# Kernel tuning notes

Hardware: AMD Instinct MI355X
Metric: run time of the kernel (lower is better)

Reference implementation:

```python
import jax, jax.numpy as jnp
import numpy as np

HEADS = 16
D_MODEL = 1024
IMG_MODEL = 512
D_K = D_MODEL // HEADS


def setup_inputs() -> dict:
    key = jax.random.key(0)
    ks = jax.random.split(key, 12)
    B, LQ, LKV = 8, 2048, 1024
    s_dm = 1.0 / np.sqrt(D_MODEL)
    s_im = 1.0 / np.sqrt(IMG_MODEL)
    return {
        "q": jax.random.normal(ks[0], (B, LQ, D_MODEL), jnp.float32),
        "k": jax.random.normal(ks[1], (B, LKV, IMG_MODEL), jnp.float32),
        "v": jax.random.normal(ks[2], (B, LKV, IMG_MODEL), jnp.float32),
        "Wq": jax.random.normal(ks[3], (D_MODEL, D_MODEL), jnp.float32) * s_dm,
        "bq": jnp.zeros((D_MODEL,), jnp.float32),
        "Wk": jax.random.normal(ks[4], (IMG_MODEL, D_MODEL), jnp.float32) * s_im,
        "bk": jnp.zeros((D_MODEL,), jnp.float32),
        "Wv": jax.random.normal(ks[5], (IMG_MODEL, D_MODEL), jnp.float32) * s_im,
        "bv": jnp.zeros((D_MODEL,), jnp.float32),
        "Wo": jax.random.normal(ks[6], (D_MODEL, D_MODEL), jnp.float32) * s_dm,
        "bo": jnp.zeros((D_MODEL,), jnp.float32),
    }


def reference(q, k, v, Wq, bq, Wk, bk, Wv, bv, Wo, bo):
    B, LQ, _ = q.shape
    LKV = k.shape[1]
    # projections -> [B, H, L, d_k]
    qh = (q @ Wq + bq).reshape(B, LQ, HEADS, D_K).transpose(0, 2, 1, 3)
    kh = (k @ Wk + bk).reshape(B, LKV, HEADS, D_K).transpose(0, 2, 1, 3)
    vh = (v @ Wv + bv).reshape(B, LKV, HEADS, D_K).transpose(0, 2, 1, 3)
    scale = 1.0 / np.sqrt(D_K)
    scores = jnp.einsum("bhqd,bhkd->bhqk", qh, kh) * scale  # [B,H,LQ,LKV]
    attn = jax.nn.softmax(scores, axis=-1)  # dropout = identity at eval
    out = jnp.einsum("bhqk,bhkd->bhqd", attn, vh)  # [B,H,LQ,d_k]
    concat = out.transpose(0, 2, 1, 3).reshape(B, LQ, D_MODEL)
    return concat @ Wo + bo
```

## Files before the change

kernel.cpp:

```cpp
#include <hip/hip_runtime.h>

typedef __bf16 bf16;
typedef __bf16 bf16x8 __attribute__((ext_vector_type(8)));
typedef __bf16 bf16x4 __attribute__((ext_vector_type(4)));
typedef float f32x4 __attribute__((ext_vector_type(4)));

constexpr int BB   = 8;
constexpr int LQ   = 2048;
constexpr int LKV  = 1024;
constexpr int DM   = 1024;
constexpr int DIMG = 512;
constexpr int H    = 16;
constexpr int DK   = 64;

__device__ inline void async16(const bf16* g, bf16* l) {
  __builtin_amdgcn_global_load_lds((const __attribute__((address_space(1))) void*)g,
                                   (__attribute__((address_space(3))) void*)l, 16, 0, 0);
}
__device__ inline float fexp2(float x) { return __builtin_amdgcn_exp2f(x); }

__global__ __launch_bounds__(256) void prep_all(const float* __restrict__ q,
                                                const float* __restrict__ k,
                                                const float* __restrict__ v,
                                                bf16* __restrict__ qo,
                                                bf16* __restrict__ ko,
                                                bf16* __restrict__ vo,
                                                int nq4, int nk4, int NC,
                                                const float* __restrict__ Wq,
                                                const float* __restrict__ Wk,
                                                const float* __restrict__ Wv,
                                                const float* __restrict__ Wo,
                                                bf16* __restrict__ WqT,
                                                bf16* __restrict__ WkT,
                                                bf16* __restrict__ WvT,
                                                bf16* __restrict__ WoT) {
  __shared__ float tile[64][65];
  const int bid = blockIdx.x;
  if (bid < NC) {
    int i = bid * 256 + threadIdx.x;
    const float* in;
    bf16* out;
    int idx;
    if (i < nq4) { in = q; out = qo; idx = i; }
    else if (i < nq4 + nk4) { in = k; out = ko; idx = i - nq4; }
    else if (i < nq4 + 2 * nk4) { in = v; out = vo; idx = i - nq4 - nk4; }
    else return;
    const float4 f = ((const float4*)in)[idx];
    bf16x4 o;
    o[0] = (bf16)f.x; o[1] = (bf16)f.y; o[2] = (bf16)f.z; o[3] = (bf16)f.w;
    ((bf16x4*)out)[idx] = o;
    return;
  }
  const int tbid = bid - NC;
  const int bx = tbid & 15, by = (tbid >> 4) & 15, z = tbid >> 8;
  const float* W;
  bf16* WT;
  int K;
  if (z == 0) { W = Wq; WT = WqT; K = DM; }
  else if (z == 1) { W = Wk; WT = WkT; K = DIMG; }
  else if (z == 2) { W = Wv; WT = WvT; K = DIMG; }
  else { W = Wo; WT = WoT; K = DM; }
  const int N = DM;
  if (bx * 64 >= K) return;

  const int k0 = bx * 64, n0 = by * 64;
  const int tx = threadIdx.x & 63, tg = threadIdx.x >> 6;
#pragma unroll
  for (int i = 0; i < 16; ++i) {
    int row = tg * 16 + i;
    tile[row][tx] = W[(size_t)(k0 + row) * N + n0 + tx];
  }
  __syncthreads();
#pragma unroll
  for (int i = 0; i < 16; ++i) {
    int nrow = tg * 16 + i;
    WT[(size_t)(n0 + nrow) * K + k0 + tx] = (bf16)tile[tx][nrow];
  }
}

template <typename OutT, bool VT_OUT>
__device__ __forceinline__ void gemm_body(const bf16* __restrict__ A,
                                          const bf16* __restrict__ Bt,
                                          const float* __restrict__ bias,
                                          OutT* __restrict__ C,
                                          int N, int K, float oscale, int bm, int bn,
                                          bf16* As, bf16* Bs) {
  const int tid = threadIdx.x, lane = tid & 63, wave = tid >> 6;
  const int wm = (wave & 1) * 64, wn = (wave >> 1) * 64;
  const int fm = lane & 15, quad = lane >> 4, fk8 = quad * 8;
  constexpr int SLOT = 128 * 32;

  f32x4 acc[4][4];
#pragma unroll
  for (int i = 0; i < 4; ++i)
#pragma unroll
    for (int j = 0; j < 4; ++j) {
      f32x4 z = {0.f, 0.f, 0.f, 0.f};
      acc[i][j] = z;
    }

  const int srow = lane >> 2, scol = (lane & 3) * 8;
  const bf16* ag0 = A + (size_t)(bm * 128 + wave * 16 + srow) * K + scol;
  const bf16* ag1 = ag0 + (size_t)64 * K;
  const bf16* bg0 = Bt + (size_t)(bn * 128 + wave * 16 + srow) * K + scol;
  const bf16* bg1 = bg0 + (size_t)64 * K;
  bf16* la0 = As + (wave * 16) * 32;
  bf16* la1 = As + (64 + wave * 16) * 32;
  bf16* lb0 = Bs + (wave * 16) * 32;
  bf16* lb1 = Bs + (64 + wave * 16) * 32;

  auto stage = [&](int t, int slot) {
    const int k0 = t * 32, so = slot * SLOT;
    async16(ag0 + k0, la0 + so);
    async16(ag1 + k0, la1 + so);
    async16(bg0 + k0, lb0 + so);
    async16(bg1 + k0, lb1 + so);
  };

  const int KT = K >> 5;
  stage(0, 0);
  stage(1, 1);

  for (int t = 0; t < KT; ++t) {
    asm volatile("s_waitcnt vmcnt(4)" ::: "memory");
    __builtin_amdgcn_s_barrier();
    __builtin_amdgcn_sched_barrier(0);
    {
      const int nt = t + 2;
      if (nt < KT) stage(nt, nt % 3);
      else if (nt == KT) stage(KT - 1, nt % 3);
    }
    const int cur = (t % 3) * SLOT;
    bf16x8 af[4], bfr[4];
#pragma unroll
    for (int i = 0; i < 4; ++i)
      af[i] = *(const bf16x8*)&As[cur + (wm + i * 16 + fm) * 32 + fk8];
#pragma unroll
    for (int j = 0; j < 4; ++j)
      bfr[j] = *(const bf16x8*)&Bs[cur + (wn + j * 16 + fm) * 32 + fk8];
#pragma unroll
    for (int i = 0; i < 4; ++i)
#pragma unroll
      for (int j = 0; j < 4; ++j)
        acc[i][j] = __builtin_amdgcn_mfma_f32_16x16x32_bf16(af[i], bfr[j], acc[i][j], 0, 0, 0);
  }
  asm volatile("s_waitcnt vmcnt(0)" ::: "memory");

#pragma unroll
  for (int j = 0; j < 4; ++j) {
    const int col = bn * 128 + wn + j * 16 + fm;
    const float bv = bias[col];
    if constexpr (VT_OUT) {
      const int h = col >> 6, dk = col & 63;
#pragma unroll
      for (int i = 0; i < 4; ++i) {
        const int row = bm * 128 + wm + i * 16 + quad * 4;
        const int b = row >> 10, t = row & 1023;
        bf16x4 o;
#pragma unroll
        for (int r = 0; r < 4; ++r) o[r] = (bf16)((acc[i][j][r] + bv) * oscale);
        *(bf16x4*)&C[(((size_t)(b * H + h) * DK + dk) << 10) + t] = o;
      }
    } else {
#pragma unroll
      for (int i = 0; i < 4; ++i) {
#pragma unroll
        for (int r = 0; r < 4; ++r) {
          const int row = bm * 128 + wm + i * 16 + quad * 4 + r;
          C[(size_t)row * N + col] = (OutT)((acc[i][j][r] + bv) * oscale);
        }
      }
    }
  }
}

template <typename OutT>
__global__ __launch_bounds__(256) void gemm_one(const bf16* __restrict__ A,
                                                const bf16* __restrict__ Bt,
                                                const float* __restrict__ bias,
                                                OutT* __restrict__ C,
                                                int N, int K, float oscale) {
  __shared__ __align__(16) bf16 As[3 * 128 * 32];
  __shared__ __align__(16) bf16 Bs[3 * 128 * 32];
  const int cpx = gridDim.x >> 3;
  const int wg = ((int)blockIdx.x & 7) * cpx + ((int)blockIdx.x >> 3);
  const int nbn = N >> 7;
  gemm_body<OutT, false>(A, Bt, bias, C, N, K, oscale, wg / nbn, wg % nbn, As, Bs);
}

__global__ __launch_bounds__(256) void gemm_qkv(const bf16* __restrict__ qbf,
                                                const bf16* __restrict__ WqT,
                                                const float* __restrict__ bq,
                                                bf16* __restrict__ qh,
                                                const bf16* __restrict__ kbf,
                                                const bf16* __restrict__ WkT,
                                                const float* __restrict__ bk,
                                                bf16* __restrict__ kh,
                                                const bf16* __restrict__ vbf,
                                                const bf16* __restrict__ WvT,
                                                const float* __restrict__ bv,
                                                bf16* __restrict__ Vt,
                                                float qscale) {
  __shared__ __align__(16) bf16 As[3 * 128 * 32];
  __shared__ __align__(16) bf16 Bs[3 * 128 * 32];
  const int cpx = gridDim.x >> 3;
  const int wg = ((int)blockIdx.x & 7) * cpx + ((int)blockIdx.x >> 3);
  if (wg < 1024) {
    gemm_body<bf16, false>(qbf, WqT, bq, qh, DM, DM, qscale, wg >> 3, wg & 7, As, Bs);
  } else if (wg < 1536) {
    const int idx = wg - 1024;
    gemm_body<bf16, false>(kbf, WkT, bk, kh, DM, DIMG, 1.0f, idx >> 3, idx & 7, As, Bs);
  } else {
    const int idx = wg - 1536;
    gemm_body<bf16, true>(vbf, WvT, bv, Vt, DM, DIMG, 1.0f, idx >> 3, idx & 7, As, Bs);
  }
}

__global__ __launch_bounds__(512, 4) void attn_kernel(const bf16* __restrict__ qh,
                                                      const bf16* __restrict__ kh,
                                                      const bf16* __restrict__ vt,
                                                      bf16* __restrict__ out) {
  constexpr int NT = LKV / 64;
  __shared__ __align__(16) bf16 Ks[2][64 * 64];
  __shared__ __align__(16) bf16 Vs[2][64 * 64];
  __shared__ __align__(16) bf16 Ps[8][32 * 64];

  const int tid = threadIdx.x, lane = tid & 63, w = tid >> 6;
  const int fm = lane & 15, quad = lane >> 4;
  const int qt = blockIdx.x, h = blockIdx.y, b = blockIdx.z;
  const int q0 = qt * 256;

  const bf16* qbase = qh + ((size_t)(b * LQ) + q0 + w * 32) * DM + h * DK;
  const bf16* kbase = kh + (size_t)(b * LKV) * DM + h * DK;
  const bf16* vbase = vt + (size_t)(b * H + h) * DK * LKV;

  bf16x8 qf[2][2];
#pragma unroll
  for (int i = 0; i < 2; ++i)
#pragma unroll
    for (int kg = 0; kg < 2; ++kg)
      qf[i][kg] = *(const bf16x8*)&qbase[(size_t)(i * 16 + fm) * DM + kg * 32 + quad * 8];

  const int srow = lane >> 3, sslot = lane & 7;
  const int fs = fm & 7;

  auto stage = [&](int t, int bf) {
    const int r0 = w * 8;
    const int row = r0 + srow;
    const int gs = (sslot ^ (row & 7)) << 3;
    async16(kbase + (size_t)(t * 64 + row) * DM + gs, &Ks[bf][r0 * 64]);
    async16(vbase + (size_t)row * LKV + t * 64 + gs, &Vs[bf][r0 * 64]);
  };

  stage(0, 0);
  stage(1, 1);

  float row_m[2] = {-1e30f, -1e30f}, row_l[2] = {0.f, 0.f};
  f32x4 o_acc[2][4];
#pragma unroll
  for (int i = 0; i < 2; ++i)
#pragma unroll
    for (int jd = 0; jd < 4; ++jd) {
      f32x4 z = {0.f, 0.f, 0.f, 0.f};
      o_acc[i][jd] = z;
    }

  bf16* Pw = Ps[w];

#pragma unroll 2
  for (int t = 0; t < NT; ++t) {
    asm volatile("s_waitcnt vmcnt(2)" ::: "memory");
    __builtin_amdgcn_s_barrier();
    __builtin_amdgcn_sched_barrier(0);
    const bf16* Kb = Ks[t & 1];
    const bf16* Vb = Vs[t & 1];

    f32x4 s[4][2];
#pragma unroll
    for (int m = 0; m < 4; ++m)
#pragma unroll
      for (int i = 0; i < 2; ++i) {
        f32x4 z = {0.f, 0.f, 0.f, 0.f};
        s[m][i] = z;
      }
    __builtin_amdgcn_s_setprio(1);
#pragma unroll
    for (int kg = 0; kg < 2; ++kg)
#pragma unroll
      for (int m = 0; m < 4; ++m) {
        const bf16x8 kf =
            *(const bf16x8*)&Kb[(m * 16 + fm) * 64 + (((kg * 4 + quad) ^ fs) << 3)];
#pragma unroll
        for (int i = 0; i < 2; ++i)
          s[m][i] = __builtin_amdgcn_mfma_f32_16x16x32_bf16(kf, qf[i][kg], s[m][i], 0, 0, 0);
      }
    __builtin_amdgcn_s_setprio(0);

#pragma unroll
    for (int i = 0; i < 2; ++i) {
      float pm[4];
#pragma unroll
      for (int m = 0; m < 4; ++m)
        pm[m] = fmaxf(fmaxf(fmaxf(s[m][i][0], s[m][i][1]), s[m][i][2]), s[m][i][3]);
      float mt = fmaxf(fmaxf(fmaxf(pm[0], pm[1]), pm[2]), pm[3]);
      mt = fmaxf(mt, __shfl_xor(mt, 16));
      mt = fmaxf(mt, __shfl_xor(mt, 32));
      float alpha = 1.f;
      if (!__all(mt <= row_m[i] + 8.0f)) {
        const float nm = fmaxf(row_m[i], mt);
        alpha = fexp2(row_m[i] - nm);
        row_m[i] = nm;
#pragma unroll
        for (int r = 0; r < 4; ++r) {
          const float a_o = __shfl(alpha, quad * 4 + r);
#pragma unroll
          for (int jd = 0; jd < 4; ++jd) o_acc[i][jd][r] *= a_o;
        }
      }
      const float mi = row_m[i];
      float pp[4];
#pragma unroll
      for (int m = 0; m < 4; ++m) {
#pragma unroll
        for (int r = 0; r < 4; ++r) s[m][i][r] = fexp2(s[m][i][r] - mi);
        pp[m] = (s[m][i][0] + s[m][i][1]) + (s[m][i][2] + s[m][i][3]);
      }
      float ps = (pp[0] + pp[1]) + (pp[2] + pp[3]);
      ps += __shfl_xor(ps, 16);
      ps += __shfl_xor(ps, 32);
      row_l[i] = row_l[i] * alpha + ps;
    }

#pragma unroll
    for (int i = 0; i < 2; ++i)
#pragma unroll
      for (int m = 0; m < 4; ++m) {
        bf16x4 p4;
#pragma unroll
        for (int r = 0; r < 4; ++r) p4[r] = (bf16)s[m][i][r];
        *(bf16x4*)&Pw[(i * 16 + fm) * 64 + (((m * 2 + (quad >> 1)) ^ fs) << 3) +
                      ((quad & 1) << 2)] = p4;
      }

    __builtin_amdgcn_s_setprio(1);
#pragma unroll
    for (int kg = 0; kg < 2; ++kg) {
      bf16x8 pf[2];
#pragma unroll
      for (int i = 0; i < 2; ++i)
        pf[i] = *(const bf16x8*)&Pw[(i * 16 + fm) * 64 + (((kg * 4 + quad) ^ fs) << 3)];
#pragma unroll
      for (int jd = 0; jd < 4; ++jd) {
        const bf16x8 vfr =
            *(const bf16x8*)&Vb[(jd * 16 + fm) * 64 + (((kg * 4 + quad) ^ fs) << 3)];
#pragma unroll
        for (int i = 0; i < 2; ++i)
          o_acc[i][jd] = __builtin_amdgcn_mfma_f32_16x16x32_bf16(pf[i], vfr, o_acc[i][jd], 0, 0, 0);
      }
    }
    __builtin_amdgcn_s_setprio(0);

    __builtin_amdgcn_sched_barrier(0);
    __builtin_amdgcn_s_barrier();
    __builtin_amdgcn_sched_barrier(0);
    if (t < NT - 1) {
      const int tn = (t + 2 < NT) ? (t + 2) : (NT - 1);
      stage(tn, t & 1);
    }
  }
  asm volatile("s_waitcnt vmcnt(0)" ::: "memory");

  const float linv0 = 1.0f / row_l[0], linv1 = 1.0f / row_l[1];
  bf16* obase = out + ((size_t)(b * LQ) + q0 + w * 32) * DM + h * DK;
#pragma unroll
  for (int i = 0; i < 2; ++i) {
    const float li = i ? linv1 : linv0;
#pragma unroll
    for (int r = 0; r < 4; ++r) {
      const float lo = __shfl(li, quad * 4 + r);
#pragma unroll
      for (int jd = 0; jd < 4; ++jd)
        obase[(size_t)(i * 16 + quad * 4 + r) * DM + jd * 16 + fm] =
            (bf16)(o_acc[i][jd][r] * lo);
    }
  }
}

extern "C" void kernel_launch(void* const* d_in, const int* in_sizes, int n_in,
                              void* d_out, int out_size, void* d_ws, size_t ws_size,
                              hipStream_t stream) {
  const float* q  = (const float*)d_in[0];
  const float* k  = (const float*)d_in[1];
  const float* v  = (const float*)d_in[2];
  const float* Wq = (const float*)d_in[3];
  const float* bq = (const float*)d_in[4];
  const float* Wk = (const float*)d_in[5];
  const float* bk = (const float*)d_in[6];
  const float* Wv = (const float*)d_in[7];
  const float* bv = (const float*)d_in[8];
  const float* Wo = (const float*)d_in[9];
  const float* bo = (const float*)d_in[10];
  float* out = (float*)d_out;

  char* ws = (char*)d_ws;
  size_t off = 0;
  auto alloc = [&](size_t bytes) -> void* {
    void* p = ws + off;
    off += (bytes + 255) & ~(size_t)255;
    return p;
  };

  const size_t nq = (size_t)BB * LQ * DM;
  const size_t nk = (size_t)BB * LKV * DIMG;
  const size_t nkh = (size_t)BB * LKV * DM;

  bf16* qbf = (bf16*)alloc(nq * 2);
  bf16* kbf = (bf16*)alloc(nk * 2);
  bf16* vbf = (bf16*)alloc(nk * 2);
  bf16* WqT = (bf16*)alloc((size_t)DM * DM * 2);
  bf16* WkT = (bf16*)alloc((size_t)DM * DIMG * 2);
  bf16* WvT = (bf16*)alloc((size_t)DM * DIMG * 2);
  bf16* WoT = (bf16*)alloc((size_t)DM * DM * 2);
  bf16* qh  = (bf16*)alloc(nq * 2);
  bf16* kh  = (bf16*)alloc(nkh * 2);
  bf16* Vt  = (bf16*)alloc(nkh * 2);
  bf16* attn_out = qbf;

  const int nq4 = (int)(nq / 4), nk4 = (int)(nk / 4);
  const int NC = (nq4 + 2 * nk4 + 255) / 256;
  prep_all<<<NC + 1024, 256, 0, stream>>>(q, k, v, qbf, kbf, vbf, nq4, nk4, NC,
                                          Wq, Wk, Wv, Wo, WqT, WkT, WvT, WoT);

  const float QSCALE = 0.125f * 1.44269504f;
  gemm_qkv<<<2048, 256, 0, stream>>>(qbf, WqT, bq, qh,
                                     kbf, WkT, bk, kh,
                                     vbf, WvT, bv, Vt, QSCALE);

  attn_kernel<<<dim3(LQ / 256, H, BB), 512, 0, stream>>>(qh, kh, Vt, attn_out);

  gemm_one<float><<<(BB * LQ / 128) * (DM / 128), 256, 0, stream>>>(
      attn_out, WoT, bo, out, DM, DM, 1.0f);
}
```

Before: 416.5 us.

## Keep softmax probabilities in registers via permlane swap; simplify GEMM pipeline to double buffer

The attention kernel no longer writes P tiles to shared memory and reads them back. Probabilities are packed to bf16 with v_cvt_pk_bf16_f32 and rearranged across lanes with permlane32_swap to form the MFMA A-operand, and V fragments are loaded as matching 8-byte pieces. This removes the Ps LDS buffer and its traffic, which may raise occupancy. Separately, the GEMM goes from a 3-stage async pipeline with waitcnt control to a 2-buffer scheme with __syncthreads each iteration, which cuts LDS use but may expose more load latency.

```diff
diff --git a/kernel.cpp b/kernel.cpp
--- a/kernel.cpp
+++ b/kernel.cpp
@@ -4,6 +4,9 @@
 typedef __bf16 bf16x8 __attribute__((ext_vector_type(8)));
 typedef __bf16 bf16x4 __attribute__((ext_vector_type(4)));
 typedef float f32x4 __attribute__((ext_vector_type(4)));
+typedef unsigned int u32;
+typedef unsigned int u32x2 __attribute__((ext_vector_type(2)));
+typedef unsigned int u32x4 __attribute__((ext_vector_type(4)));
 
 constexpr int BB   = 8;
 constexpr int LQ   = 2048;
@@ -18,6 +21,11 @@
                                    (__attribute__((address_space(3))) void*)l, 16, 0, 0);
 }
 __device__ inline float fexp2(float x) { return __builtin_amdgcn_exp2f(x); }
+__device__ inline u32 cvtpk(float lo, float hi) {
+  u32 r;
+  asm("v_cvt_pk_bf16_f32 %0, %1, %2" : "=v"(r) : "v"(lo), "v"(hi));
+  return r;
+}
 
 __global__ __launch_bounds__(256) void prep_all(const float* __restrict__ q,
                                                 const float* __restrict__ k,
@@ -109,28 +117,23 @@
   bf16* lb0 = Bs + (wave * 16) * 32;
   bf16* lb1 = Bs + (64 + wave * 16) * 32;
 
-  auto stage = [&](int t, int slot) {
-    const int k0 = t * 32, so = slot * SLOT;
-    async16(ag0 + k0, la0 + so);
-    async16(ag1 + k0, la1 + so);
-    async16(bg0 + k0, lb0 + so);
-    async16(bg1 + k0, lb1 + so);
-  };
-
   const int KT = K >> 5;
-  stage(0, 0);
-  stage(1, 1);
+  async16(ag0, la0);
+  async16(ag1, la1);
+  async16(bg0, lb0);
+  async16(bg1, lb1);
+  __syncthreads();
 
   for (int t = 0; t < KT; ++t) {
-    asm volatile("s_waitcnt vmcnt(4)" ::: "memory");
-    __builtin_amdgcn_s_barrier();
-    __builtin_amdgcn_sched_barrier(0);
-    {
-      const int nt = t + 2;
-      if (nt < KT) stage(nt, nt % 3);
-      else if (nt == KT) stage(KT - 1, nt % 3);
-    }
-    const int cur = (t % 3) * SLOT;
+    const int cur = (t & 1) * SLOT;
+    if (t + 1 < KT) {
+      const int nxt = ((t + 1) & 1) * SLOT;
+      const int k0 = (t + 1) * 32;
+      async16(ag0 + k0, la0 + nxt);
+      async16(ag1 + k0, la1 + nxt);
+      async16(bg0 + k0, lb0 + nxt);
+      async16(bg1 + k0, lb1 + nxt);
+    }
     bf16x8 af[4], bfr[4];
 #pragma unroll
     for (int i = 0; i < 4; ++i)
@@ -143,8 +146,8 @@
 #pragma unroll
       for (int j = 0; j < 4; ++j)
         acc[i][j] = __builtin_amdgcn_mfma_f32_16x16x32_bf16(af[i], bfr[j], acc[i][j], 0, 0, 0);
-  }
-  asm volatile("s_waitcnt vmcnt(0)" ::: "memory");
+    __syncthreads();
+  }
 
 #pragma unroll
   for (int j = 0; j < 4; ++j) {
@@ -180,8 +183,8 @@
                                                 const float* __restrict__ bias,
                                                 OutT* __restrict__ C,
                                                 int N, int K, float oscale) {
-  __shared__ __align__(16) bf16 As[3 * 128 * 32];
-  __shared__ __align__(16) bf16 Bs[3 * 128 * 32];
+  __shared__ __align__(16) bf16 As[2 * 128 * 32];
+  __shared__ __align__(16) bf16 Bs[2 * 128 * 32];
   const int cpx = gridDim.x >> 3;
   const int wg = ((int)blockIdx.x & 7) * cpx + ((int)blockIdx.x >> 3);
   const int nbn = N >> 7;
@@ -201,8 +204,8 @@
                                                 const float* __restrict__ bv,
                                                 bf16* __restrict__ Vt,
                                                 float qscale) {
-  __shared__ __align__(16) bf16 As[3 * 128 * 32];
-  __shared__ __align__(16) bf16 Bs[3 * 128 * 32];
+  __shared__ __align__(16) bf16 As[2 * 128 * 32];
+  __shared__ __align__(16) bf16 Bs[2 * 128 * 32];
   const int cpx = gridDim.x >> 3;
   const int wg = ((int)blockIdx.x & 7) * cpx + ((int)blockIdx.x >> 3);
   if (wg < 1024) {
@@ -223,7 +226,6 @@
   constexpr int NT = LKV / 64;
   __shared__ __align__(16) bf16 Ks[2][64 * 64];
   __shared__ __align__(16) bf16 Vs[2][64 * 64];
-  __shared__ __align__(16) bf16 Ps[8][32 * 64];
 
   const int tid = threadIdx.x, lane = tid & 63, w = tid >> 6;
   const int fm = lane & 15, quad = lane >> 4;
@@ -265,7 +267,7 @@
       o_acc[i][jd] = z;
     }
 
-  bf16* Pw = Ps[w];
+  const int gb = ((quad >> 1) << 4) + ((quad & 1) << 2);
 
 #pragma unroll 2
   for (int t = 0; t < NT; ++t) {
@@ -331,28 +333,30 @@
       row_l[i] = row_l[i] * alpha + ps;
     }
 
-#pragma unroll
-    for (int i = 0; i < 2; ++i)
-#pragma unroll
-      for (int m = 0; m < 4; ++m) {
-        bf16x4 p4;
-#pragma unroll
-        for (int r = 0; r < 4; ++r) p4[r] = (bf16)s[m][i][r];
-        *(bf16x4*)&Pw[(i * 16 + fm) * 64 + (((m * 2 + (quad >> 1)) ^ fs) << 3) +
-                      ((quad & 1) << 2)] = p4;
-      }
-
     __builtin_amdgcn_s_setprio(1);
 #pragma unroll
     for (int kg = 0; kg < 2; ++kg) {
       bf16x8 pf[2];
 #pragma unroll
-      for (int i = 0; i < 2; ++i)
-        pf[i] = *(const bf16x8*)&Pw[(i * 16 + fm) * 64 + (((kg * 4 + quad) ^ fs) << 3)];
+      for (int i = 0; i < 2; ++i) {
+        const u32 a1 = cvtpk(s[2 * kg][i][0], s[2 * kg][i][1]);
+        const u32 a2 = cvtpk(s[2 * kg][i][2], s[2 * kg][i][3]);
+        const u32 b1 = cvtpk(s[2 * kg + 1][i][0], s[2 * kg + 1][i][1]);
+        const u32 b2 = cvtpk(s[2 * kg + 1][i][2], s[2 * kg + 1][i][3]);
+        const u32x2 r1 = __builtin_amdgcn_permlane32_swap(a1, b1, false, false);
+        const u32x2 r2 = __builtin_amdgcn_permlane32_swap(a2, b2, false, false);
+        const u32x4 pw = {r1[0], r2[0], r1[1], r2[1]};
+        pf[i] = __builtin_bit_cast(bf16x8, pw);
+      }
+      const int g1 = kg * 32 + gb;
+      const int g2 = g1 + 8;
 #pragma unroll
       for (int jd = 0; jd < 4; ++jd) {
-        const bf16x8 vfr =
-            *(const bf16x8*)&Vb[(jd * 16 + fm) * 64 + (((kg * 4 + quad) ^ fs) << 3)];
+        const int vr = jd * 16 + fm;
+        const u32x2 vlo = *(const u32x2*)&Vb[vr * 64 + (((g1 >> 3) ^ fs) << 3) + (g1 & 7)];
+        const u32x2 vhi = *(const u32x2*)&Vb[vr * 64 + (((g2 >> 3) ^ fs) << 3) + (g2 & 7)];
+        const u32x4 wv = {vlo[0], vlo[1], vhi[0], vhi[1]};
+        const bf16x8 vfr = __builtin_bit_cast(bf16x8, wv);
 #pragma unroll
         for (int i = 0; i < 2; ++i)
           o_acc[i][jd] = __builtin_amdgcn_mfma_f32_16x16x32_bf16(pf[i], vfr, o_acc[i][jd], 0, 0, 0);
```

Result: no change. 412.3 us (-1.0%).
